# Kernel tuning notes

Measured on AMD Instinct MI355X. Metric: run time of the kernel, lower is better.

## Reference

```python
import jax, jax.numpy as jnp
import numpy as np

EPS = 1e-5
NUM_MEM_TOKENS = 16
SEGMENT_SIZE = 512


def dpfp(x):
    # DPFP feature map (Schlag et al.), nu=1: doubles the last dim, all-nonnegative.
    x2 = jnp.concatenate([jax.nn.relu(x), jax.nn.relu(-x)], axis=-1)
    return x2 * jnp.roll(x2, 1, axis=-1)


def setup_inputs() -> dict:
    key = jax.random.key(0)
    ks = jax.random.split(key, 7)
    B, S, D, DM = 4, 4224, 1024, 64  # S = n_seg * (segment_size + num_mem_tokens) = 8*528
    scale = 0.02
    return {
        "hidden_states": jax.random.normal(ks[0], (B, S, D), jnp.float32),
        "model_output": jax.random.normal(ks[1], (B, S, D), jnp.float32),
        "W_mq": jax.random.normal(ks[2], (D, DM), jnp.float32) * scale,
        "W_mk": jax.random.normal(ks[3], (D, DM), jnp.float32) * scale,
        "W_mv": jax.random.normal(ks[4], (D, D), jnp.float32) * scale,
        "W_mb": jax.random.normal(ks[5], (D, D), jnp.float32) * scale,
        "b_mb": jnp.zeros((D,), jnp.float32),
    }


def reference(hidden_states, model_output, W_mq, W_mk, W_mv, W_mb, b_mb):
    B, S, D = hidden_states.shape
    L = SEGMENT_SIZE + NUM_MEM_TOKENS
    n_seg = S // L
    d_key = 2 * W_mq.shape[1]  # dpfp doubles feature dim

    # [n_seg, B, L, D]
    h = hidden_states.reshape(B, n_seg, L, D).transpose(1, 0, 2, 3)
    m = model_output.reshape(B, n_seg, L, D).transpose(1, 0, 2, 3)

    def step(carry, seg):
        W_mem, z = carry  # [B, d_key, D], [B, d_key]
        hid, mo = seg     # [B, L, D] each
        # --- associate: linear-attention read of compressive memory ---
        q = dpfp(hid @ W_mq)                                   # [B, L, d_key]
        num = jnp.einsum('blk,bkd->bld', q, W_mem)             # [B, L, D]
        den = jnp.einsum('blk,bk->bl', q, z)[..., None] + EPS
        assoc = num / den
        # --- delta-rule memory update from memory tokens of segment output ---
        mem = (assoc + mo)[:, -NUM_MEM_TOKENS:]                # [B, M, D]
        k = dpfp(mem @ W_mk)                                   # [B, M, d_key]
        v = mem @ W_mv                                         # [B, M, D]
        gate = jax.nn.sigmoid(mem @ W_mb + b_mb)               # [B, M, D]
        prev = jnp.einsum('bmk,bkd->bmd', k, W_mem) / (
            jnp.einsum('bmk,bk->bm', k, z)[..., None] + EPS)   # correction (old value)
        new_info = gate * (v - prev)
        W_mem = W_mem + jnp.einsum('bmk,bmd->bkd', k, new_info)
        z = z + k.sum(axis=1)
        return (W_mem, z), assoc

    W0 = jnp.zeros((B, d_key, D), hidden_states.dtype)
    z0 = jnp.zeros((B, d_key), hidden_states.dtype)
    _, assocs = jax.lax.scan(step, (W0, z0), (h, m))           # [n_seg, B, L, D]
    association = jnp.tanh(assocs.transpose(1, 0, 2, 3).reshape(B, S, D))
    return model_output + association
```

## Files before the change

### kernel.cpp

```cpp
#include <hip/hip_runtime.h>
#include <hip/hip_bf16.h>

#define EPS 1e-5f
#define NBLK 64

typedef short s8v __attribute__((ext_vector_type(8)));
typedef short s4v __attribute__((ext_vector_type(4)));
typedef float f4v __attribute__((ext_vector_type(4)));

__device__ __forceinline__ unsigned short f2bf(float f) {
  unsigned u = __builtin_bit_cast(unsigned, f);
  u = u + 0x7FFFu + ((u >> 16) & 1u);
  return (unsigned short)(u >> 16);
}
__device__ __forceinline__ float bf2f(unsigned short h) {
  unsigned u = ((unsigned)h) << 16;
  return __builtin_bit_cast(float, u);
}
__device__ __forceinline__ float fast_tanh(float x) {
  float e = __expf(2.0f * x);
  return 1.0f - 2.0f / (e + 1.0f);
}
__device__ __forceinline__ float fast_sigmoid(float x) {
  return 1.0f / (1.0f + __expf(-x));
}
__device__ __forceinline__ float frcp(float x) { return __builtin_amdgcn_rcpf(x); }

__global__ __launch_bounds__(256) void transpose_kernel(
    const float* __restrict__ W_mq, const float* __restrict__ W_mk,
    const float* __restrict__ W_mv, const float* __restrict__ W_mb,
    unsigned short* __restrict__ W_mqT, unsigned short* __restrict__ W_mkT,
    unsigned short* __restrict__ W_mvT, unsigned short* __restrict__ W_mbT) {
  __shared__ float tile[32][33];
  int bid = blockIdx.x;
  const float* src; unsigned short* dst; int N, t0;
  if (bid < 64)        { src = W_mq; dst = W_mqT; N = 64;   t0 = bid; }
  else if (bid < 128)  { src = W_mk; dst = W_mkT; N = 64;   t0 = bid - 64; }
  else if (bid < 1152) { src = W_mv; dst = W_mvT; N = 1024; t0 = bid - 128; }
  else                 { src = W_mb; dst = W_mbT; N = 1024; t0 = bid - 1152; }
  const int K = 1024;
  int tk = t0 & 31, tn = t0 >> 5;
  int k0 = tk * 32, n0 = tn * 32;
  int t = threadIdx.x;
  int cr = t >> 5, cc = t & 31;
#pragma unroll
  for (int u = 0; u < 4; u++) {
    int row = cr + u * 8;
    tile[row][cc] = src[(size_t)(k0 + row) * N + n0 + cc];
  }
  __syncthreads();
#pragma unroll
  for (int u = 0; u < 4; u++) {
    int nl = cr + u * 8;
    dst[(size_t)(n0 + nl) * K + k0 + cc] = f2bf(tile[cc][nl]);
  }
}

__global__ __launch_bounds__(128) void q_kernel(
    const float* __restrict__ HS, const unsigned short* __restrict__ W_mqT,
    unsigned short* __restrict__ Q) {
  __shared__ __align__(16) union { float y[16 * 64]; unsigned short kq[16 * 128]; } lds;
  int t = threadIdx.x, wv = t >> 6, lane = t & 63, m = lane & 15, q = lane >> 4;
  int r0 = blockIdx.x * 16;
  const float* ap = HS + (size_t)(r0 + m) * 1024 + wv * 512 + q * 8;
  const unsigned short* bp = W_mqT + (size_t)m * 1024 + wv * 512 + q * 8;
  f4v acc[4] = {f4v{0,0,0,0}, f4v{0,0,0,0}, f4v{0,0,0,0}, f4v{0,0,0,0}};
#pragma unroll 4
  for (int ks = 0; ks < 16; ks++) {
    int k0 = ks * 32;
    f4v h0 = *(const f4v*)(ap + k0);
    f4v h1 = *(const f4v*)(ap + k0 + 4);
    s8v a;
    a[0] = (short)f2bf(h0[0]); a[1] = (short)f2bf(h0[1]);
    a[2] = (short)f2bf(h0[2]); a[3] = (short)f2bf(h0[3]);
    a[4] = (short)f2bf(h1[0]); a[5] = (short)f2bf(h1[1]);
    a[6] = (short)f2bf(h1[2]); a[7] = (short)f2bf(h1[3]);
#pragma unroll
    for (int nf = 0; nf < 4; nf++) {
      s8v b = *(const s8v*)(bp + nf * 16384 + k0);
      acc[nf] = __builtin_amdgcn_mfma_f32_16x16x32_bf16(a, b, acc[nf], 0, 0, 0);
    }
  }
  if (wv == 1) {
#pragma unroll
    for (int nf = 0; nf < 4; nf++)
#pragma unroll
      for (int i = 0; i < 4; i++)
        lds.y[(nf * 4 + i) * 64 + lane] = acc[nf][i];
  }
  __syncthreads();
  if (wv == 0) {
#pragma unroll
    for (int nf = 0; nf < 4; nf++)
#pragma unroll
      for (int i = 0; i < 4; i++)
        acc[nf][i] += lds.y[(nf * 4 + i) * 64 + lane];
    int srcl = (lane & 48) | ((m + 15) & 15);
#pragma unroll
    for (int i = 0; i < 4; i++) {
      float yp[4];
#pragma unroll
      for (int nf = 0; nf < 4; nf++) yp[nf] = __shfl(acc[nf][i], srcl);
      int r = q * 4 + i;
#pragma unroll
      for (int nf = 0; nf < 4; nf++) {
        float yv = acc[nf][i];
        float py = (m != 0) ? yp[nf] : (nf > 0 ? yp[nf - 1] : yp[3]);
        bool wrap = (m == 0 && nf == 0);
        float x2lo = wrap ? fmaxf(-py, 0.f) : fmaxf(py, 0.f);
        float x2hi = wrap ? fmaxf(py, 0.f) : fmaxf(-py, 0.f);
        lds.kq[r * 128 + nf * 16 + m]      = f2bf(fmaxf(yv, 0.f) * x2lo);
        lds.kq[r * 128 + 64 + nf * 16 + m] = f2bf(fmaxf(-yv, 0.f) * x2hi);
      }
    }
  }
  __syncthreads();
  {
    int row = t >> 3, ch = t & 7;
    unsigned short* qp = Q + (size_t)(r0 + row) * 128 + ch * 16;
    *(s8v*)(qp)     = *(const s8v*)&lds.kq[row * 128 + ch * 16];
    *(s8v*)(qp + 8) = *(const s8v*)&lds.kq[row * 128 + ch * 16 + 8];
  }
}

__global__ __launch_bounds__(256, 1) void scan_kernel(
    const unsigned short* __restrict__ Qb, const unsigned short* __restrict__ W_mkT,
    const unsigned short* __restrict__ W_mvT, const unsigned short* __restrict__ W_mbT,
    const float* __restrict__ b_mb, const float* __restrict__ MO,
    float* __restrict__ OUT, unsigned short* __restrict__ hist,
    float* __restrict__ zh, unsigned short* __restrict__ mem_bf, int* bar) {
  __shared__ float Wf[128 * 64];
  __shared__ __align__(16) unsigned short Wbf[64 * 132];
  __shared__ __align__(16) unsigned short mem_l[16 * 1032];
  __shared__ float y_lds[16 * 64];
  __shared__ __align__(16) float k_f[16 * 128];
  __shared__ __align__(16) unsigned short k_bf[16 * 128];
  __shared__ float part[256];
  __shared__ float kden_l[16];
  __shared__ float ni_lds[16 * 65];
  __shared__ float z_l[128];

  int t = threadIdx.x, wv = t >> 6, lane = t & 63, m = lane & 15, q = lane >> 4;
  int ct = blockIdx.x & 15, b = blockIdx.x >> 4;

  for (int i = t; i < 128 * 64; i += 256) Wf[i] = 0.f;
  for (int i = t; i < 64 * 132; i += 256) Wbf[i] = 0;
  if (t < 128) z_l[t] = 0.f;
  __syncthreads();

  for (int s = 0; s < 8; s++) {
    {
      int col = t >> 2, koff = (t & 3) * 32;
      const unsigned short* srcp = &Wbf[col * 132 + koff];
      unsigned short* dstp = hist + (size_t)s * 524288 +
                             ((size_t)b * 1024 + ct * 64 + col) * 128 + koff;
#pragma unroll
      for (int u = 0; u < 4; u++) *(s8v*)(dstp + u * 8) = *(const s8v*)(srcp + u * 8);
      if (ct == 0 && t < 128) zh[s * 512 + b * 128 + t] = z_l[t];
    }
    {
      size_t grow = (size_t)b * 4224 + s * 528 + 512;
      const unsigned short* qp = Qb + (grow + m) * 128;
      s8v a[4];
      float dp = 0.f;
#pragma unroll
      for (int ks = 0; ks < 4; ks++) {
        a[ks] = *(const s8v*)(qp + ks * 32 + q * 8);
#pragma unroll
        for (int j = 0; j < 8; j++)
          dp += bf2f((unsigned short)a[ks][j]) * z_l[ks * 32 + q * 8 + j];
      }
      dp += __shfl_xor(dp, 16);
      dp += __shfl_xor(dp, 32);
      dp += EPS;
      f4v acc = {0, 0, 0, 0};
#pragma unroll
      for (int ks = 0; ks < 4; ks++) {
        s8v bv = *(const s8v*)&Wbf[(wv * 16 + m) * 132 + ks * 32 + q * 8];
        acc = __builtin_amdgcn_mfma_f32_16x16x32_bf16(a[ks], bv, acc, 0, 0, 0);
      }
      unsigned short* mb = mem_bf + (s & 1) * 65536;
#pragma unroll
      for (int i = 0; i < 4; i++) {
        float rden = frcp(__shfl(dp, q * 4 + i));
        int col = ct * 64 + wv * 16 + m;
        size_t rbase = (grow + q * 4 + i) * 1024;
        float assoc = acc[i] * rden;
        float mov = MO[rbase + col];
        OUT[rbase + col] = mov + fast_tanh(assoc);
        mb[(size_t)(b * 16 + q * 4 + i) * 1024 + col] = f2bf(assoc + mov);
      }
    }
    __syncthreads();
    if (t == 0) {
      __threadfence();
      atomicAdd(bar + s, 1);
      while (atomicAdd(bar + s, 0) < NBLK) __builtin_amdgcn_s_sleep(2);
      __threadfence();
    }
    __syncthreads();
    {
      const unsigned short* srcp = mem_bf + (s & 1) * 65536 + b * 16384;
      int r = t >> 4, c0 = (t & 15) * 64;
#pragma unroll
      for (int u = 0; u < 8; u++)
        *(s8v*)&mem_l[r * 1032 + c0 + u * 8] = *(const s8v*)(srcp + r * 1024 + c0 + u * 8);
    }
    __syncthreads();
    {
      const unsigned short* ap2 = &mem_l[m * 1032];
      const unsigned short* bp = W_mkT + (size_t)(wv * 16 + m) * 1024;
      f4v acy = {0, 0, 0, 0};
      for (int ks = 0; ks < 32; ks++) {
        s8v av = *(const s8v*)(ap2 + ks * 32 + q * 8);
        s8v bv = *(const s8v*)(bp + ks * 32 + q * 8);
        acy = __builtin_amdgcn_mfma_f32_16x16x32_bf16(av, bv, acy, 0, 0, 0);
      }
#pragma unroll
      for (int i = 0; i < 4; i++) y_lds[(q * 4 + i) * 64 + wv * 16 + m] = acy[i];
    }
    __syncthreads();
    {
      int r = t >> 4, jg = t & 15;
      const float* yr = &y_lds[r * 64];
      float pd = 0.f;
#pragma unroll
      for (int u = 0; u < 8; u++) {
        int jj = jg * 8 + u, jm = (jj + 127) & 127;
        float yj = (jj < 64) ? yr[jj] : -yr[jj - 64];
        float ym = (jm < 64) ? yr[jm] : -yr[jm - 64];
        float kv = fmaxf(yj, 0.f) * fmaxf(ym, 0.f);
        k_f[r * 128 + jj] = kv;
        k_bf[r * 128 + jj] = f2bf(kv);
        pd += kv * z_l[jj];
      }
      part[t] = pd;
    }
    __syncthreads();
    if (t < 16) {
      float ssum = 0.f;
#pragma unroll
      for (int jg = 0; jg < 16; jg++) ssum += part[t * 16 + jg];
      kden_l[t] = ssum + EPS;
    }
    __syncthreads();
    {
      int c = ct * 64 + wv * 16 + m;
      const unsigned short* ap2 = &mem_l[m * 1032];
      const unsigned short* bvp = W_mvT + (size_t)c * 1024;
      const unsigned short* bgp = W_mbT + (size_t)c * 1024;
      f4v accv = {0,0,0,0}, accg = {0,0,0,0}, accp = {0,0,0,0};
      for (int ks = 0; ks < 32; ks++) {
        s8v av = *(const s8v*)(ap2 + ks * 32 + q * 8);
        s8v bv = *(const s8v*)(bvp + ks * 32 + q * 8);
        s8v bg = *(const s8v*)(bgp + ks * 32 + q * 8);
        accv = __builtin_amdgcn_mfma_f32_16x16x32_bf16(av, bv, accv, 0, 0, 0);
        accg = __builtin_amdgcn_mfma_f32_16x16x32_bf16(av, bg, accg, 0, 0, 0);
      }
#pragma unroll
      for (int ks = 0; ks < 4; ks++) {
        s8v ak = *(const s8v*)&k_bf[m * 128 + ks * 32 + q * 8];
        s8v bm = *(const s8v*)&Wbf[(wv * 16 + m) * 132 + ks * 32 + q * 8];
        accp = __builtin_amdgcn_mfma_f32_16x16x32_bf16(ak, bm, accp, 0, 0, 0);
      }
      float bmb = b_mb[c];
#pragma unroll
      for (int i = 0; i < 4; i++) {
        int r = q * 4 + i;
        float prev = accp[i] * frcp(kden_l[r]);
        float g = fast_sigmoid(accg[i] + bmb);
        ni_lds[r * 65 + wv * 16 + m] = g * (accv[i] - prev);
      }
    }
    __syncthreads();
    {
      int cl = t & 63, kg = t >> 6;
      float niv[16];
#pragma unroll
      for (int mm = 0; mm < 16; mm++) niv[mm] = ni_lds[mm * 65 + cl];
      float delta[32];
#pragma unroll
      for (int jj = 0; jj < 32; jj++) delta[jj] = 0.f;
#pragma unroll
      for (int mm = 0; mm < 16; mm++) {
        const float* kb = &k_f[mm * 128 + kg * 32];
        float nv = niv[mm];
#pragma unroll
        for (int ch = 0; ch < 8; ch++) {
          f4v kv4 = *(const f4v*)(kb + ch * 4);
#pragma unroll
          for (int jj = 0; jj < 4; jj++) delta[ch * 4 + jj] += kv4[jj] * nv;
        }
      }
#pragma unroll
      for (int c8 = 0; c8 < 4; c8++) {
        s8v pk;
#pragma unroll
        for (int u = 0; u < 8; u++) {
          int kk = kg * 32 + c8 * 8 + u;
          float nv = Wf[kk * 64 + cl] + delta[c8 * 8 + u];
          Wf[kk * 64 + cl] = nv;
          pk[u] = (short)f2bf(nv);
        }
        *(s8v*)&Wbf[cl * 132 + kg * 32 + c8 * 8] = pk;
      }
      if (t < 128) {
        float ssum = 0.f;
#pragma unroll
        for (int r = 0; r < 16; r++) ssum += k_f[r * 128 + t];
        z_l[t] += ssum;
      }
    }
    __syncthreads();
  }
}

__global__ __launch_bounds__(256) void a_bulk_kernel(
    const unsigned short* __restrict__ Qb, const unsigned short* __restrict__ hist,
    const float* __restrict__ zh, const float* __restrict__ MO,
    float* __restrict__ OUT) {
  __shared__ float as_l[64 * 65];
  int t = threadIdx.x, wv = t >> 6, lane = t & 63, m = lane & 15, q = lane >> 4;
  int rt4 = blockIdx.x, ct = blockIdx.y;
  int seg = blockIdx.z >> 2, b = blockIdx.z & 3;
  const unsigned short* Wm = hist + (size_t)seg * 524288 + ((size_t)b * 1024 + ct * 64) * 128;
  const float* zp = zh + seg * 512 + b * 128;
  size_t grow = (size_t)b * 4224 + seg * 528 + rt4 * 64 + wv * 16;
  const unsigned short* qp = Qb + (grow + m) * 128;
  s8v a[4];
  float dp = 0.f;
#pragma unroll
  for (int ks = 0; ks < 4; ks++) {
    a[ks] = *(const s8v*)(qp + ks * 32 + q * 8);
    f4v z0 = *(const f4v*)(zp + ks * 32 + q * 8);
    f4v z1 = *(const f4v*)(zp + ks * 32 + q * 8 + 4);
#pragma unroll
    for (int j = 0; j < 4; j++) dp += bf2f((unsigned short)a[ks][j]) * z0[j];
#pragma unroll
    for (int j = 0; j < 4; j++) dp += bf2f((unsigned short)a[ks][j + 4]) * z1[j];
  }
  dp += __shfl_xor(dp, 16);
  dp += __shfl_xor(dp, 32);
  dp += EPS;
  f4v acc[4] = {f4v{0,0,0,0}, f4v{0,0,0,0}, f4v{0,0,0,0}, f4v{0,0,0,0}};
#pragma unroll
  for (int ks = 0; ks < 4; ks++) {
#pragma unroll
    for (int nf = 0; nf < 4; nf++) {
      s8v bv = *(const s8v*)(Wm + (size_t)(nf * 16 + m) * 128 + ks * 32 + q * 8);
      acc[nf] = __builtin_amdgcn_mfma_f32_16x16x32_bf16(a[ks], bv, acc[nf], 0, 0, 0);
    }
  }
#pragma unroll
  for (int i = 0; i < 4; i++) {
    float rden = frcp(__shfl(dp, q * 4 + i));
#pragma unroll
    for (int nf = 0; nf < 4; nf++)
      as_l[(wv * 16 + q * 4 + i) * 65 + nf * 16 + m] = acc[nf][i] * rden;
  }
  __syncthreads();
  {
    int r = t >> 2, cchunk = (t & 3) * 16;
    size_t rbase = ((size_t)b * 4224 + seg * 528 + rt4 * 64 + r) * 1024 + ct * 64 + cchunk;
    const float* ar = &as_l[r * 65 + cchunk];
#pragma unroll
    for (int u = 0; u < 4; u++) {
      f4v mo = *(const f4v*)(MO + rbase + u * 4);
      f4v o;
#pragma unroll
      for (int j = 0; j < 4; j++) o[j] = mo[j] + fast_tanh(ar[u * 4 + j]);
      *(f4v*)(OUT + rbase + u * 4) = o;
    }
  }
}

extern "C" void kernel_launch(void* const* d_in, const int* in_sizes, int n_in,
                              void* d_out, int out_size, void* d_ws, size_t ws_size,
                              hipStream_t stream) {
  const float* HS  = (const float*)d_in[0];
  const float* MO  = (const float*)d_in[1];
  const float* W_mq = (const float*)d_in[2];
  const float* W_mk = (const float*)d_in[3];
  const float* W_mv = (const float*)d_in[4];
  const float* W_mb = (const float*)d_in[5];
  const float* b_mb = (const float*)d_in[6];
  float* OUT = (float*)d_out;

  char* wsb = (char*)d_ws;
  unsigned short* hist   = (unsigned short*)(wsb + 0);
  float*          zh     = (float*)(wsb + 8388608);
  unsigned short* Qb     = (unsigned short*)(wsb + 8404992);
  unsigned short* W_mqT  = (unsigned short*)(wsb + 12730368);
  unsigned short* W_mkT  = (unsigned short*)(wsb + 12861440);
  unsigned short* W_mvT  = (unsigned short*)(wsb + 12992512);
  unsigned short* W_mbT  = (unsigned short*)(wsb + 15089664);
  unsigned short* mem_bf = (unsigned short*)(wsb + 17186816);
  int*            bar    = (int*)(wsb + 17448960);

  (void)hipMemsetAsync(bar, 0, 64, stream);
  transpose_kernel<<<2176, 256, 0, stream>>>(W_mq, W_mk, W_mv, W_mb,
                                             W_mqT, W_mkT, W_mvT, W_mbT);
  q_kernel<<<1056, 128, 0, stream>>>(HS, W_mqT, Qb);
  scan_kernel<<<NBLK, 256, 0, stream>>>(Qb, W_mkT, W_mvT, W_mbT, b_mb, MO, OUT,
                                        hist, zh, mem_bf, bar);
  a_bulk_kernel<<<dim3(8, 16, 32), 256, 0, stream>>>(Qb, hist, zh, MO, OUT);
}
```

Measured before the change: 467.1 us.

## Per-batch barriers, fused memory-token GEMMs, and prefetch in the serial scan kernel

```diff
diff --git a/kernel.cpp b/kernel.cpp
--- a/kernel.cpp
+++ b/kernel.cpp
@@ -2,7 +2,6 @@
 #include <hip/hip_bf16.h>
 
 #define EPS 1e-5f
-#define NBLK 64
 
 typedef short s8v __attribute__((ext_vector_type(8)));
 typedef short s4v __attribute__((ext_vector_type(4)));
@@ -131,45 +130,41 @@
     float* __restrict__ zh, unsigned short* __restrict__ mem_bf, int* bar) {
   __shared__ float Wf[128 * 64];
   __shared__ __align__(16) unsigned short Wbf[64 * 132];
-  __shared__ __align__(16) unsigned short mem_l[16 * 1032];
   __shared__ float y_lds[16 * 64];
   __shared__ __align__(16) float k_f[16 * 128];
-  __shared__ __align__(16) unsigned short k_bf[16 * 128];
-  __shared__ float part[256];
+  __shared__ __align__(16) unsigned short k_bf[16 * 136];
   __shared__ float kden_l[16];
   __shared__ float ni_lds[16 * 65];
   __shared__ float z_l[128];
 
   int t = threadIdx.x, wv = t >> 6, lane = t & 63, m = lane & 15, q = lane >> 4;
   int ct = blockIdx.x & 15, b = blockIdx.x >> 4;
+  int col = ct * 64 + wv * 16 + m;
 
   for (int i = t; i < 128 * 64; i += 256) Wf[i] = 0.f;
   for (int i = t; i < 64 * 132; i += 256) Wbf[i] = 0;
   if (t < 128) z_l[t] = 0.f;
+  float bmb = b_mb[col];
   __syncthreads();
+
+  s8v aq[4]; float mo_pf[4];
+  {
+    const unsigned short* qp = Qb + ((size_t)b * 4224 + 512 + m) * 128;
+#pragma unroll
+    for (int ks = 0; ks < 4; ks++) aq[ks] = *(const s8v*)(qp + ks * 32 + q * 8);
+    const float* mop = MO + ((size_t)b * 4224 + 512 + q * 4) * 1024 + col;
+#pragma unroll
+    for (int i = 0; i < 4; i++) mo_pf[i] = mop[(size_t)i * 1024];
+  }
 
   for (int s = 0; s < 8; s++) {
     {
-      int col = t >> 2, koff = (t & 3) * 32;
-      const unsigned short* srcp = &Wbf[col * 132 + koff];
-      unsigned short* dstp = hist + (size_t)s * 524288 +
-                             ((size_t)b * 1024 + ct * 64 + col) * 128 + koff;
-#pragma unroll
-      for (int u = 0; u < 4; u++) *(s8v*)(dstp + u * 8) = *(const s8v*)(srcp + u * 8);
-      if (ct == 0 && t < 128) zh[s * 512 + b * 128 + t] = z_l[t];
-    }
-    {
-      size_t grow = (size_t)b * 4224 + s * 528 + 512;
-      const unsigned short* qp = Qb + (grow + m) * 128;
-      s8v a[4];
       float dp = 0.f;
 #pragma unroll
-      for (int ks = 0; ks < 4; ks++) {
-        a[ks] = *(const s8v*)(qp + ks * 32 + q * 8);
+      for (int ks = 0; ks < 4; ks++)
 #pragma unroll
         for (int j = 0; j < 8; j++)
-          dp += bf2f((unsigned short)a[ks][j]) * z_l[ks * 32 + q * 8 + j];
-      }
+          dp += bf2f((unsigned short)aq[ks][j]) * z_l[ks * 32 + q * 8 + j];
       dp += __shfl_xor(dp, 16);
       dp += __shfl_xor(dp, 32);
       dp += EPS;
@@ -177,44 +172,45 @@
 #pragma unroll
       for (int ks = 0; ks < 4; ks++) {
         s8v bv = *(const s8v*)&Wbf[(wv * 16 + m) * 132 + ks * 32 + q * 8];
-        acc = __builtin_amdgcn_mfma_f32_16x16x32_bf16(a[ks], bv, acc, 0, 0, 0);
-      }
-      unsigned short* mb = mem_bf + (s & 1) * 65536;
+        acc = __builtin_amdgcn_mfma_f32_16x16x32_bf16(aq[ks], bv, acc, 0, 0, 0);
+      }
+      unsigned short* mb = mem_bf + (s & 1) * 65536 + b * 16384;
+      size_t grow = (size_t)b * 4224 + s * 528 + 512;
 #pragma unroll
       for (int i = 0; i < 4; i++) {
         float rden = frcp(__shfl(dp, q * 4 + i));
-        int col = ct * 64 + wv * 16 + m;
-        size_t rbase = (grow + q * 4 + i) * 1024;
         float assoc = acc[i] * rden;
-        float mov = MO[rbase + col];
-        OUT[rbase + col] = mov + fast_tanh(assoc);
-        mb[(size_t)(b * 16 + q * 4 + i) * 1024 + col] = f2bf(assoc + mov);
+        float mov = mo_pf[i];
+        OUT[(grow + q * 4 + i) * 1024 + col] = mov + fast_tanh(assoc);
+        mb[(q * 4 + i) * 1024 + col] = f2bf(assoc + mov);
       }
     }
     __syncthreads();
     if (t == 0) {
       __threadfence();
-      atomicAdd(bar + s, 1);
-      while (atomicAdd(bar + s, 0) < NBLK) __builtin_amdgcn_s_sleep(2);
+      atomicAdd(bar + s * 4 + b, 1);
+      while (__hip_atomic_load(bar + s * 4 + b, __ATOMIC_RELAXED,
+                               __HIP_MEMORY_SCOPE_AGENT) < 16)
+        __builtin_amdgcn_s_sleep(1);
       __threadfence();
     }
     __syncthreads();
+    f4v accv = {0,0,0,0}, accg = {0,0,0,0};
     {
-      const unsigned short* srcp = mem_bf + (s & 1) * 65536 + b * 16384;
-      int r = t >> 4, c0 = (t & 15) * 64;
-#pragma unroll
-      for (int u = 0; u < 8; u++)
-        *(s8v*)&mem_l[r * 1032 + c0 + u * 8] = *(const s8v*)(srcp + r * 1024 + c0 + u * 8);
-    }
-    __syncthreads();
-    {
-      const unsigned short* ap2 = &mem_l[m * 1032];
-      const unsigned short* bp = W_mkT + (size_t)(wv * 16 + m) * 1024;
+      const unsigned short* avp = mem_bf + (s & 1) * 65536 + b * 16384 + m * 1024 + q * 8;
+      const unsigned short* bkp = W_mkT + (size_t)(wv * 16 + m) * 1024 + q * 8;
+      const unsigned short* bvp = W_mvT + (size_t)col * 1024 + q * 8;
+      const unsigned short* bgp = W_mbT + (size_t)col * 1024 + q * 8;
       f4v acy = {0, 0, 0, 0};
+#pragma unroll 4
       for (int ks = 0; ks < 32; ks++) {
-        s8v av = *(const s8v*)(ap2 + ks * 32 + q * 8);
-        s8v bv = *(const s8v*)(bp + ks * 32 + q * 8);
-        acy = __builtin_amdgcn_mfma_f32_16x16x32_bf16(av, bv, acy, 0, 0, 0);
+        s8v av = *(const s8v*)(avp + ks * 32);
+        s8v bk = *(const s8v*)(bkp + ks * 32);
+        s8v bv = *(const s8v*)(bvp + ks * 32);
+        s8v bg = *(const s8v*)(bgp + ks * 32);
+        acy  = __builtin_amdgcn_mfma_f32_16x16x32_bf16(av, bk, acy, 0, 0, 0);
+        accv = __builtin_amdgcn_mfma_f32_16x16x32_bf16(av, bv, accv, 0, 0, 0);
+        accg = __builtin_amdgcn_mfma_f32_16x16x32_bf16(av, bg, accg, 0, 0, 0);
       }
 #pragma unroll
       for (int i = 0; i < 4; i++) y_lds[(q * 4 + i) * 64 + wv * 16 + m] = acy[i];
@@ -231,39 +227,24 @@
         float ym = (jm < 64) ? yr[jm] : -yr[jm - 64];
         float kv = fmaxf(yj, 0.f) * fmaxf(ym, 0.f);
         k_f[r * 128 + jj] = kv;
-        k_bf[r * 128 + jj] = f2bf(kv);
+        k_bf[r * 136 + jj] = f2bf(kv);
         pd += kv * z_l[jj];
       }
-      part[t] = pd;
-    }
-    __syncthreads();
-    if (t < 16) {
-      float ssum = 0.f;
-#pragma unroll
-      for (int jg = 0; jg < 16; jg++) ssum += part[t * 16 + jg];
-      kden_l[t] = ssum + EPS;
+      pd += __shfl_xor(pd, 1);
+      pd += __shfl_xor(pd, 2);
+      pd += __shfl_xor(pd, 4);
+      pd += __shfl_xor(pd, 8);
+      if (jg == 0) kden_l[r] = pd + EPS;
     }
     __syncthreads();
     {
-      int c = ct * 64 + wv * 16 + m;
-      const unsigned short* ap2 = &mem_l[m * 1032];
-      const unsigned short* bvp = W_mvT + (size_t)c * 1024;
-      const unsigned short* bgp = W_mbT + (size_t)c * 1024;
-      f4v accv = {0,0,0,0}, accg = {0,0,0,0}, accp = {0,0,0,0};
-      for (int ks = 0; ks < 32; ks++) {
-        s8v av = *(const s8v*)(ap2 + ks * 32 + q * 8);
-        s8v bv = *(const s8v*)(bvp + ks * 32 + q * 8);
-        s8v bg = *(const s8v*)(bgp + ks * 32 + q * 8);
-        accv = __builtin_amdgcn_mfma_f32_16x16x32_bf16(av, bv, accv, 0, 0, 0);
-        accg = __builtin_amdgcn_mfma_f32_16x16x32_bf16(av, bg, accg, 0, 0, 0);
-      }
+      f4v accp = {0, 0, 0, 0};
 #pragma unroll
       for (int ks = 0; ks < 4; ks++) {
-        s8v ak = *(const s8v*)&k_bf[m * 128 + ks * 32 + q * 8];
+        s8v ak = *(const s8v*)&k_bf[m * 136 + ks * 32 + q * 8];
         s8v bm = *(const s8v*)&Wbf[(wv * 16 + m) * 132 + ks * 32 + q * 8];
         accp = __builtin_amdgcn_mfma_f32_16x16x32_bf16(ak, bm, accp, 0, 0, 0);
       }
-      float bmb = b_mb[c];
 #pragma unroll
       for (int i = 0; i < 4; i++) {
         int r = q * 4 + i;
@@ -271,6 +252,13 @@
         float g = fast_sigmoid(accg[i] + bmb);
         ni_lds[r * 65 + wv * 16 + m] = g * (accv[i] - prev);
       }
+      if (t < 128) {
+        float ssum = 0.f;
+#pragma unroll
+        for (int r = 0; r < 16; r++) ssum += k_f[r * 128 + t];
+        z_l[t] += ssum;
+        if (s < 7) zh[(s + 1) * 512 + b * 128 + t] = z_l[t];
+      }
     }
     __syncthreads();
     {
@@ -292,6 +280,8 @@
           for (int jj = 0; jj < 4; jj++) delta[ch * 4 + jj] += kv4[jj] * nv;
         }
       }
+      unsigned short* hdst = hist + (size_t)(s + 1) * 524288 +
+                             ((size_t)b * 1024 + ct * 64 + cl) * 128 + kg * 32;
 #pragma unroll
       for (int c8 = 0; c8 < 4; c8++) {
         s8v pk;
@@ -303,12 +293,15 @@
           pk[u] = (short)f2bf(nv);
         }
         *(s8v*)&Wbf[cl * 132 + kg * 32 + c8 * 8] = pk;
-      }
-      if (t < 128) {
-        float ssum = 0.f;
-#pragma unroll
-        for (int r = 0; r < 16; r++) ssum += k_f[r * 128 + t];
-        z_l[t] += ssum;
+        if (s < 7) *(s8v*)(hdst + c8 * 8) = pk;
+      }
+      if (s < 7) {
+        const unsigned short* qp = Qb + ((size_t)b * 4224 + (s + 1) * 528 + 512 + m) * 128;
+#pragma unroll
+        for (int ks = 0; ks < 4; ks++) aq[ks] = *(const s8v*)(qp + ks * 32 + q * 8);
+        const float* mop = MO + ((size_t)b * 4224 + (s + 1) * 528 + 512 + q * 4) * 1024 + col;
+#pragma unroll
+        for (int i = 0; i < 4; i++) mo_pf[i] = mop[(size_t)i * 1024];
       }
     }
     __syncthreads();
@@ -397,11 +390,13 @@
   unsigned short* mem_bf = (unsigned short*)(wsb + 17186816);
   int*            bar    = (int*)(wsb + 17448960);
 
-  (void)hipMemsetAsync(bar, 0, 64, stream);
+  (void)hipMemsetAsync(wsb, 0, 1048576, stream);
+  (void)hipMemsetAsync(wsb + 8388608, 0, 2048, stream);
+  (void)hipMemsetAsync(bar, 0, 128, stream);
   transpose_kernel<<<2176, 256, 0, stream>>>(W_mq, W_mk, W_mv, W_mb,
                                              W_mqT, W_mkT, W_mvT, W_mbT);
   q_kernel<<<1056, 128, 0, stream>>>(HS, W_mqT, Qb);
-  scan_kernel<<<NBLK, 256, 0, stream>>>(Qb, W_mkT, W_mvT, W_mbT, b_mb, MO, OUT,
-                                        hist, zh, mem_bf, bar);
+  scan_kernel<<<64, 256, 0, stream>>>(Qb, W_mkT, W_mvT, W_mbT, b_mb, MO, OUT,
+                                      hist, zh, mem_bf, bar);
   a_bulk_kernel<<<dim3(8, 16, 32), 256, 0, stream>>>(Qb, hist, zh, MO, OUT);
 }
```

New measurement: 464.9 us. About the same (-0.5%).
